# Performance work log

Hardware: AMD Instinct MI355X
Metric: run time of the kernel (lower is better)

Reference implementation:

```python
import jax, jax.numpy as jnp
import numpy as np

B, TE, TD, HE, HD = 4, 512, 256, 128, 256

def setup_inputs() -> dict:
    key = jax.random.key(0)
    k1, k2, k3, k4, k5 = jax.random.split(key, 5)
    return {
        "encoder_out_seq": jax.random.normal(k1, (B, TE, HE), dtype=jnp.float32),
        "decoder_out_seq": jax.random.normal(k2, (B, TD, HD), dtype=jnp.float32),
        "W_a": jax.random.normal(k3, (HE, HE), dtype=jnp.float32) * 0.05,
        "U_a": jax.random.normal(k4, (HD, HE), dtype=jnp.float32) * 0.05,
        "V_a": jax.random.normal(k5, (HE, 1), dtype=jnp.float32) * 0.05,
    }

def reference(encoder_out_seq, decoder_out_seq, W_a, U_a, V_a):
    # Bahdanau additive attention, fully parallel over decoder steps
    # (the original K.rnn scan has no true recurrence: each step is independent).
    Ws = jnp.einsum('bse,ef->bsf', encoder_out_seq, W_a)   # [B,Te,He]
    Uh = jnp.einsum('btd,df->btf', decoder_out_seq, U_a)   # [B,Td,He]
    # [B,Td,Te,He] additive score features
    feat = jnp.tanh(Ws[:, None, :, :] + Uh[:, :, None, :])
    e = jnp.einsum('btsf,f->bts', feat, V_a[:, 0])         # [B,Td,Te]
    e = jax.nn.softmax(e, axis=-1)                         # attention weights
    c = jnp.einsum('bts,bse->bte', e, encoder_out_seq)     # [B,Td,He] contexts
    return (c, e)
```

## Files before the change

### kernel.cpp

```cpp
#include <hip/hip_runtime.h>

#define Bn  4
#define TEn 512
#define TDn 256
#define HEn 128
#define HDn 256

#define KSCALE 2.8853900817779268f
#define LOG2E  1.4426950408889634f

#if __has_builtin(__builtin_amdgcn_exp2f)
#define EXP2(x) __builtin_amdgcn_exp2f(x)
#else
#define EXP2(x) __expf(0.6931471805599453f * (x))
#endif

__device__ __forceinline__ float sigEP(float E, float P) {
    return __builtin_amdgcn_rcpf(fmaf(E, P, 1.0f));
}

__global__ __launch_bounds__(512) void proj_kernel(
    const float* __restrict__ enc, const float* __restrict__ dec,
    const float* __restrict__ W, const float* __restrict__ U,
    float* __restrict__ Ew, float* __restrict__ P)
{
    const int tid = threadIdx.x;
    if (blockIdx.x < 512) {
        __shared__ __align__(16) float enc_lds[4 * HEn];
        const int c  = tid & (HEn - 1);
        const int rl = tid >> 7;
        const int r0 = blockIdx.x * 4;
        enc_lds[tid] = enc[r0 * HEn + tid];
        __syncthreads();
        const float* wc = W + c;
        const float* er = enc_lds + rl * HEn;
        float acc = 0.f;
        #pragma unroll 4
        for (int k = 0; k < HEn; k += 8) {
            float4 e0 = *(const float4*)(er + k);
            float4 e1 = *(const float4*)(er + k + 4);
            acc = fmaf(e0.x, wc[(k + 0) * HEn], acc);
            acc = fmaf(e0.y, wc[(k + 1) * HEn], acc);
            acc = fmaf(e0.z, wc[(k + 2) * HEn], acc);
            acc = fmaf(e0.w, wc[(k + 3) * HEn], acc);
            acc = fmaf(e1.x, wc[(k + 4) * HEn], acc);
            acc = fmaf(e1.y, wc[(k + 5) * HEn], acc);
            acc = fmaf(e1.z, wc[(k + 6) * HEn], acc);
            acc = fmaf(e1.w, wc[(k + 7) * HEn], acc);
        }
        Ew[(r0 + rl) * HEn + c] = EXP2(acc * KSCALE);
    } else {
        __shared__ __align__(16) float dec_lds[4 * HDn];
        __shared__ __align__(16) float part[4][512];
        const int bt0 = (blockIdx.x - 512) * 4;
        dec_lds[tid]       = dec[bt0 * HDn + tid];
        dec_lds[tid + 512] = dec[bt0 * HDn + tid + 512];
        __syncthreads();
        const int f = tid & 127;
        const int p = tid >> 7;
        const float* u = U + (p * 64) * HEn + f;
        float a0 = 0.f, a1 = 0.f, a2 = 0.f, a3 = 0.f;
        #pragma unroll 8
        for (int k = 0; k < 64; ++k) {
            const float uk = u[k * HEn];
            const int kk = p * 64 + k;
            a0 = fmaf(dec_lds[kk],            uk, a0);
            a1 = fmaf(dec_lds[HDn + kk],      uk, a1);
            a2 = fmaf(dec_lds[2 * HDn + kk],  uk, a2);
            a3 = fmaf(dec_lds[3 * HDn + kk],  uk, a3);
        }
        part[p][f]       = a0;
        part[p][128 + f] = a1;
        part[p][256 + f] = a2;
        part[p][384 + f] = a3;
        __syncthreads();
        const int r = tid >> 7;
        const float s = part[0][r * 128 + f] + part[1][r * 128 + f]
                      + part[2][r * 128 + f] + part[3][r * 128 + f];
        P[(bt0 + r) * HEn + f] = EXP2(s * KSCALE);
    }
}

__global__ __launch_bounds__(1024, 4) void attn_kernel(
    const float* __restrict__ enc, const float* __restrict__ V,
    const float* __restrict__ Ew, const float* __restrict__ P,
    float* __restrict__ c_out, float* __restrict__ e_out)
{
    const int b    = blockIdx.x >> 6;
    const int t0   = (blockIdx.x & 63) * 4;
    const int bt0  = b * TDn + t0;
    const int tid  = threadIdx.x;
    const int lane = tid & 63;
    const int wave = tid >> 6;

    __shared__ __align__(16) float sc[4][TEn];
    __shared__ __align__(16) float part[32][512];
    __shared__ float reds[4][8];

    {
        const int s_sub = lane & 7;
        const int f0    = (lane >> 3) * 16;
        float4 vn[4], uu[4][4];
        float sv = 0.f;
        #pragma unroll
        for (int j = 0; j < 4; ++j) {
            float4 v = *(const float4*)(V + f0 + 4 * j);
            sv += v.x + v.y + v.z + v.w;
            vn[j] = make_float4(-2.f * v.x, -2.f * v.y, -2.f * v.z, -2.f * v.w);
            #pragma unroll
            for (int r = 0; r < 4; ++r)
                uu[r][j] = *(const float4*)(P + (bt0 + r) * HEn + f0 + 4 * j);
        }
        const float* wsb = Ew + (b * TEn + wave * 32) * HEn;
        #pragma unroll
        for (int ci = 0; ci < 4; ++ci) {
            const float* wp = wsb + (ci * 8 + s_sub) * HEn + f0;
            float x0 = sv, x1 = sv, x2 = sv, x3 = sv;
            #pragma unroll
            for (int j = 0; j < 4; ++j) {
                float4 w = ((const float4*)wp)[j];
                x0 = fmaf(vn[j].x, sigEP(w.x, uu[0][j].x), x0);
                x1 = fmaf(vn[j].x, sigEP(w.x, uu[1][j].x), x1);
                x2 = fmaf(vn[j].x, sigEP(w.x, uu[2][j].x), x2);
                x3 = fmaf(vn[j].x, sigEP(w.x, uu[3][j].x), x3);
                x0 = fmaf(vn[j].y, sigEP(w.y, uu[0][j].y), x0);
                x1 = fmaf(vn[j].y, sigEP(w.y, uu[1][j].y), x1);
                x2 = fmaf(vn[j].y, sigEP(w.y, uu[2][j].y), x2);
                x3 = fmaf(vn[j].y, sigEP(w.y, uu[3][j].y), x3);
                x0 = fmaf(vn[j].z, sigEP(w.z, uu[0][j].z), x0);
                x1 = fmaf(vn[j].z, sigEP(w.z, uu[1][j].z), x1);
                x2 = fmaf(vn[j].z, sigEP(w.z, uu[2][j].z), x2);
                x3 = fmaf(vn[j].z, sigEP(w.z, uu[3][j].z), x3);
                x0 = fmaf(vn[j].w, sigEP(w.w, uu[0][j].w), x0);
                x1 = fmaf(vn[j].w, sigEP(w.w, uu[1][j].w), x1);
                x2 = fmaf(vn[j].w, sigEP(w.w, uu[2][j].w), x2);
                x3 = fmaf(vn[j].w, sigEP(w.w, uu[3][j].w), x3);
            }
            x0 += __shfl_xor(x0, 8, 64);  x1 += __shfl_xor(x1, 8, 64);
            x0 += __shfl_xor(x0, 16, 64); x1 += __shfl_xor(x1, 16, 64);
            x2 += __shfl_xor(x2, 8, 64);  x3 += __shfl_xor(x3, 8, 64);
            x2 += __shfl_xor(x2, 16, 64); x3 += __shfl_xor(x3, 16, 64);
            x0 += __shfl_xor(x0, 32, 64); x1 += __shfl_xor(x1, 32, 64);
            x2 += __shfl_xor(x2, 32, 64); x3 += __shfl_xor(x3, 32, 64);
            if (lane < 8) {
                const int s = wave * 32 + ci * 8 + lane;
                sc[0][s] = EXP2(LOG2E * x0); sc[1][s] = EXP2(LOG2E * x1);
                sc[2][s] = EXP2(LOG2E * x2); sc[3][s] = EXP2(LOG2E * x3);
            }
        }
    }
    __syncthreads();

    {
        const int s  = tid & 511;
        const int r0 = (tid >> 9) * 2;
        const int w8 = wave & 7;
        const float ex0 = sc[r0][s];
        const float ex1 = sc[r0 + 1][s];
        float s0 = ex0, s1 = ex1;
        #pragma unroll
        for (int off = 32; off; off >>= 1) {
            s0 += __shfl_xor(s0, off, 64);
            s1 += __shfl_xor(s1, off, 64);
        }
        if (lane == 0) { reds[r0][w8] = s0; reds[r0 + 1][w8] = s1; }
        __syncthreads();
        float bs0 = reds[r0][0], bs1 = reds[r0 + 1][0];
        #pragma unroll
        for (int w = 1; w < 8; ++w) { bs0 += reds[r0][w]; bs1 += reds[r0 + 1][w]; }
        const float e0 = ex0 * __builtin_amdgcn_rcpf(bs0);
        const float e1 = ex1 * __builtin_amdgcn_rcpf(bs1);
        e_out[(bt0 + r0) * TEn + s]     = e0;
        e_out[(bt0 + r0 + 1) * TEn + s] = e1;
        sc[r0][s]     = e0;
        sc[r0 + 1][s] = e1;
    }
    __syncthreads();

    {
        const int hl = tid & 31;
        const int sp = tid >> 5;
        const float* eb = enc + (b * TEn + sp * 16) * HEn + hl * 4;
        float4 a0 = {0,0,0,0}, a1 = {0,0,0,0}, a2 = {0,0,0,0}, a3 = {0,0,0,0};
        #pragma unroll 4
        for (int i = 0; i < 16; ++i) {
            const int s = sp * 16 + i;
            const float4 ev = *(const float4*)(eb + i * HEn);
            const float w0 = sc[0][s], w1 = sc[1][s];
            const float w2 = sc[2][s], w3 = sc[3][s];
            a0.x = fmaf(w0, ev.x, a0.x); a1.x = fmaf(w1, ev.x, a1.x);
            a2.x = fmaf(w2, ev.x, a2.x); a3.x = fmaf(w3, ev.x, a3.x);
            a0.y = fmaf(w0, ev.y, a0.y); a1.y = fmaf(w1, ev.y, a1.y);
            a2.y = fmaf(w2, ev.y, a2.y); a3.y = fmaf(w3, ev.y, a3.y);
            a0.z = fmaf(w0, ev.z, a0.z); a1.z = fmaf(w1, ev.z, a1.z);
            a2.z = fmaf(w2, ev.z, a2.z); a3.z = fmaf(w3, ev.z, a3.z);
            a0.w = fmaf(w0, ev.w, a0.w); a1.w = fmaf(w1, ev.w, a1.w);
            a2.w = fmaf(w2, ev.w, a2.w); a3.w = fmaf(w3, ev.w, a3.w);
        }
        *(float4*)&part[sp][0   + hl * 4] = a0;
        *(float4*)&part[sp][128 + hl * 4] = a1;
        *(float4*)&part[sp][256 + hl * 4] = a2;
        *(float4*)&part[sp][384 + hl * 4] = a3;
    }
    __syncthreads();
    if (tid < 512) {
        const int r = tid >> 7, h = tid & 127;
        float s0 = 0.f, s1 = 0.f;
        #pragma unroll
        for (int p = 0; p < 32; p += 2) {
            s0 += part[p][r * 128 + h];
            s1 += part[p + 1][r * 128 + h];
        }
        c_out[(bt0 + r) * HEn + h] = s0 + s1;
    }
}

extern "C" void kernel_launch(void* const* d_in, const int* in_sizes, int n_in,
                              void* d_out, int out_size, void* d_ws, size_t ws_size,
                              hipStream_t stream) {
    const float* enc = (const float*)d_in[0];
    const float* dec = (const float*)d_in[1];
    const float* W   = (const float*)d_in[2];
    const float* U   = (const float*)d_in[3];
    const float* V   = (const float*)d_in[4];
    float* out   = (float*)d_out;
    float* c_out = out;
    float* e_out = out + Bn * TDn * HEn;
    float* Ew    = (float*)d_ws;
    float* P     = Ew + Bn * TEn * HEn;

    proj_kernel<<<768, 512, 0, stream>>>(enc, dec, W, U, Ew, P);
    attn_kernel<<<(Bn * TDn) / 4, 1024, 0, stream>>>(enc, V, Ew, P, c_out, e_out);
}
```

Measured before the change: 85.78 us.

## Share one reciprocal across four sigmoids and fold softmax sum into score pass

The four per-row sigmoid reciprocals are merged into a single reciprocal of the product of their denominators, and the individual terms are recovered with multiplies. This cuts transcendental rcp instructions by four times in the hot score loop. LOG2E is folded into the V weights so the exp2 needs no extra scale. The softmax row sums are accumulated during the score pass, which removes a block barrier and a full-block shuffle reduction. The final context reduction becomes a two-level float4 reduction. The product of four denominators could overflow or lose precision for large exp values.

```diff
diff --git a/kernel.cpp b/kernel.cpp
--- a/kernel.cpp
+++ b/kernel.cpp
@@ -14,10 +14,6 @@
 #else
 #define EXP2(x) __expf(0.6931471805599453f * (x))
 #endif
-
-__device__ __forceinline__ float sigEP(float E, float P) {
-    return __builtin_amdgcn_rcpf(fmaf(E, P, 1.0f));
-}
 
 __global__ __launch_bounds__(512) void proj_kernel(
     const float* __restrict__ enc, const float* __restrict__ dec,
@@ -95,7 +91,8 @@
 
     __shared__ __align__(16) float sc[4][TEn];
     __shared__ __align__(16) float part[32][512];
-    __shared__ float reds[4][8];
+    __shared__ __align__(16) float4 part2[4][128];
+    __shared__ __align__(16) float reds[4][16];
 
     {
         const int s_sub = lane & 7;
@@ -106,12 +103,15 @@
         for (int j = 0; j < 4; ++j) {
             float4 v = *(const float4*)(V + f0 + 4 * j);
             sv += v.x + v.y + v.z + v.w;
-            vn[j] = make_float4(-2.f * v.x, -2.f * v.y, -2.f * v.z, -2.f * v.w);
+            const float m = -2.f * LOG2E;
+            vn[j] = make_float4(m * v.x, m * v.y, m * v.z, m * v.w);
             #pragma unroll
             for (int r = 0; r < 4; ++r)
                 uu[r][j] = *(const float4*)(P + (bt0 + r) * HEn + f0 + 4 * j);
         }
+        sv *= LOG2E;
         const float* wsb = Ew + (b * TEn + wave * 32) * HEn;
+        float ds0 = 0.f, ds1 = 0.f, ds2 = 0.f, ds3 = 0.f;
         #pragma unroll
         for (int ci = 0; ci < 4; ++ci) {
             const float* wp = wsb + (ci * 8 + s_sub) * HEn + f0;
@@ -119,22 +119,24 @@
             #pragma unroll
             for (int j = 0; j < 4; ++j) {
                 float4 w = ((const float4*)wp)[j];
-                x0 = fmaf(vn[j].x, sigEP(w.x, uu[0][j].x), x0);
-                x1 = fmaf(vn[j].x, sigEP(w.x, uu[1][j].x), x1);
-                x2 = fmaf(vn[j].x, sigEP(w.x, uu[2][j].x), x2);
-                x3 = fmaf(vn[j].x, sigEP(w.x, uu[3][j].x), x3);
-                x0 = fmaf(vn[j].y, sigEP(w.y, uu[0][j].y), x0);
-                x1 = fmaf(vn[j].y, sigEP(w.y, uu[1][j].y), x1);
-                x2 = fmaf(vn[j].y, sigEP(w.y, uu[2][j].y), x2);
-                x3 = fmaf(vn[j].y, sigEP(w.y, uu[3][j].y), x3);
-                x0 = fmaf(vn[j].z, sigEP(w.z, uu[0][j].z), x0);
-                x1 = fmaf(vn[j].z, sigEP(w.z, uu[1][j].z), x1);
-                x2 = fmaf(vn[j].z, sigEP(w.z, uu[2][j].z), x2);
-                x3 = fmaf(vn[j].z, sigEP(w.z, uu[3][j].z), x3);
-                x0 = fmaf(vn[j].w, sigEP(w.w, uu[0][j].w), x0);
-                x1 = fmaf(vn[j].w, sigEP(w.w, uu[1][j].w), x1);
-                x2 = fmaf(vn[j].w, sigEP(w.w, uu[2][j].w), x2);
-                x3 = fmaf(vn[j].w, sigEP(w.w, uu[3][j].w), x3);
+                #define SIG4(comp)                                            \
+                {                                                             \
+                    const float e_ = w.comp;                                  \
+                    float D0 = fmaf(e_, uu[0][j].comp, 1.f);                  \
+                    float D1 = fmaf(e_, uu[1][j].comp, 1.f);                  \
+                    float D2 = fmaf(e_, uu[2][j].comp, 1.f);                  \
+                    float D3 = fmaf(e_, uu[3][j].comp, 1.f);                  \
+                    float P01 = D0 * D1, P23 = D2 * D3;                       \
+                    float Q = __builtin_amdgcn_rcpf(P01 * P23);               \
+                    float t_  = vn[j].comp * Q;                               \
+                    float u01 = t_ * P23, u23 = t_ * P01;                     \
+                    x0 = fmaf(u01, D1, x0);                                   \
+                    x1 = fmaf(u01, D0, x1);                                   \
+                    x2 = fmaf(u23, D3, x2);                                   \
+                    x3 = fmaf(u23, D2, x3);                                   \
+                }
+                SIG4(x) SIG4(y) SIG4(z) SIG4(w)
+                #undef SIG4
             }
             x0 += __shfl_xor(x0, 8, 64);  x1 += __shfl_xor(x1, 8, 64);
             x0 += __shfl_xor(x0, 16, 64); x1 += __shfl_xor(x1, 16, 64);
@@ -144,8 +146,22 @@
             x2 += __shfl_xor(x2, 32, 64); x3 += __shfl_xor(x3, 32, 64);
             if (lane < 8) {
                 const int s = wave * 32 + ci * 8 + lane;
-                sc[0][s] = EXP2(LOG2E * x0); sc[1][s] = EXP2(LOG2E * x1);
-                sc[2][s] = EXP2(LOG2E * x2); sc[3][s] = EXP2(LOG2E * x3);
+                const float e0 = EXP2(x0), e1 = EXP2(x1);
+                const float e2 = EXP2(x2), e3 = EXP2(x3);
+                sc[0][s] = e0; sc[1][s] = e1; sc[2][s] = e2; sc[3][s] = e3;
+                ds0 += e0; ds1 += e1; ds2 += e2; ds3 += e3;
+            }
+        }
+        if (lane < 8) {
+            ds0 += __shfl_xor(ds0, 1, 64); ds1 += __shfl_xor(ds1, 1, 64);
+            ds2 += __shfl_xor(ds2, 1, 64); ds3 += __shfl_xor(ds3, 1, 64);
+            ds0 += __shfl_xor(ds0, 2, 64); ds1 += __shfl_xor(ds1, 2, 64);
+            ds2 += __shfl_xor(ds2, 2, 64); ds3 += __shfl_xor(ds3, 2, 64);
+            ds0 += __shfl_xor(ds0, 4, 64); ds1 += __shfl_xor(ds1, 4, 64);
+            ds2 += __shfl_xor(ds2, 4, 64); ds3 += __shfl_xor(ds3, 4, 64);
+            if (lane == 0) {
+                reds[0][wave] = ds0; reds[1][wave] = ds1;
+                reds[2][wave] = ds2; reds[3][wave] = ds3;
             }
         }
     }
@@ -154,22 +170,16 @@
     {
         const int s  = tid & 511;
         const int r0 = (tid >> 9) * 2;
-        const int w8 = wave & 7;
-        const float ex0 = sc[r0][s];
-        const float ex1 = sc[r0 + 1][s];
-        float s0 = ex0, s1 = ex1;
-        #pragma unroll
-        for (int off = 32; off; off >>= 1) {
-            s0 += __shfl_xor(s0, off, 64);
-            s1 += __shfl_xor(s1, off, 64);
-        }
-        if (lane == 0) { reds[r0][w8] = s0; reds[r0 + 1][w8] = s1; }
-        __syncthreads();
-        float bs0 = reds[r0][0], bs1 = reds[r0 + 1][0];
-        #pragma unroll
-        for (int w = 1; w < 8; ++w) { bs0 += reds[r0][w]; bs1 += reds[r0 + 1][w]; }
-        const float e0 = ex0 * __builtin_amdgcn_rcpf(bs0);
-        const float e1 = ex1 * __builtin_amdgcn_rcpf(bs1);
+        const float4* R0 = (const float4*)reds[r0];
+        const float4* R1 = (const float4*)reds[r0 + 1];
+        float4 a0 = R0[0], a1 = R0[1], a2 = R0[2], a3 = R0[3];
+        float4 b0 = R1[0], b1 = R1[1], b2 = R1[2], b3 = R1[3];
+        const float bs0 = ((a0.x + a0.y) + (a0.z + a0.w)) + ((a1.x + a1.y) + (a1.z + a1.w))
+                        + ((a2.x + a2.y) + (a2.z + a2.w)) + ((a3.x + a3.y) + (a3.z + a3.w));
+        const float bs1 = ((b0.x + b0.y) + (b0.z + b0.w)) + ((b1.x + b1.y) + (b1.z + b1.w))
+                        + ((b2.x + b2.y) + (b2.z + b2.w)) + ((b3.x + b3.y) + (b3.z + b3.w));
+        const float e0 = sc[r0][s]     * __builtin_amdgcn_rcpf(bs0);
+        const float e1 = sc[r0 + 1][s] * __builtin_amdgcn_rcpf(bs1);
         e_out[(bt0 + r0) * TEn + s]     = e0;
         e_out[(bt0 + r0 + 1) * TEn + s] = e1;
         sc[r0][s]     = e0;
@@ -204,14 +214,27 @@
     }
     __syncthreads();
     if (tid < 512) {
-        const int r = tid >> 7, h = tid & 127;
-        float s0 = 0.f, s1 = 0.f;
+        const int q  = tid & 127;
+        const int pg = tid >> 7;
+        float4 a = {0, 0, 0, 0};
         #pragma unroll
-        for (int p = 0; p < 32; p += 2) {
-            s0 += part[p][r * 128 + h];
-            s1 += part[p + 1][r * 128 + h];
-        }
-        c_out[(bt0 + r) * HEn + h] = s0 + s1;
+        for (int p = pg * 8; p < pg * 8 + 8; ++p) {
+            const float4 v = ((const float4*)&part[p][0])[q];
+            a.x += v.x; a.y += v.y; a.z += v.z; a.w += v.w;
+        }
+        part2[pg][q] = a;
+    }
+    __syncthreads();
+    if (tid < 128) {
+        const int q = tid, r = q >> 5, h4 = (q & 31) * 4;
+        const float4 a0 = part2[0][q], a1 = part2[1][q];
+        const float4 a2 = part2[2][q], a3 = part2[3][q];
+        float4 o;
+        o.x = (a0.x + a1.x) + (a2.x + a3.x);
+        o.y = (a0.y + a1.y) + (a2.y + a3.y);
+        o.z = (a0.z + a1.z) + (a2.z + a3.z);
+        o.w = (a0.w + a1.w) + (a2.w + a3.w);
+        *(float4*)&c_out[(bt0 + r) * HEn + h4] = o;
     }
 }
 
```

Result: no change. 86.31 us (+0.6%).
